# Performance work log

Measured on AMD Instinct MI355X. Metric: run time of the kernel, lower is better.

The kernel has to match this reference:

```python
import jax, jax.numpy as jnp
import numpy as np

HEADS = 4
EPS_LN = 1e-5
EPS_NORM = 1e-12

def conv1x1(x, w):
    # x: [B,C,T,H,W], w: [O,C] (Conv3d kernel_size=1, no bias)
    return jnp.einsum('oc,bcthw->bothw', w, x)

def dwconv3(x, w):
    # depthwise Conv3d 3x3x3, padding=1; w: [C,1,3,3,3]
    return jax.lax.conv_general_dilated(
        x, w, window_strides=(1, 1, 1), padding='SAME',
        dimension_numbers=('NCDHW', 'OIDHW', 'NCDHW'),
        feature_group_count=x.shape[1])

def layernorm_c(x, w, b):
    # LayerNorm over channel dim (torch LN applied after b c t h w -> b (thw) c)
    m = jnp.mean(x, axis=1, keepdims=True)
    v = jnp.mean(jnp.square(x - m), axis=1, keepdims=True)
    xn = (x - m) * jax.lax.rsqrt(v + EPS_LN)
    return xn * w[None, :, None, None, None] + b[None, :, None, None, None]

def l2norm(x):
    n = jnp.sqrt(jnp.sum(jnp.square(x), axis=-1, keepdims=True))
    return x / jnp.maximum(n, EPS_NORM)

def attention_c(x, qkv_w, qkv_dw_w, proj_w, temperature):
    B, C, T, H, W = x.shape
    qkv = dwconv3(conv1x1(x, qkv_w), qkv_dw_w)  # [B,3C,T,H,W]
    q, k, v = jnp.split(qkv, 3, axis=1)
    def to_heads(a):
        return a.reshape(B, HEADS, C // HEADS, T * H * W)  # b head c (thw)
    q, k, v = to_heads(q), to_heads(k), to_heads(v)
    q = l2norm(q)
    k = l2norm(k)
    # channel attention: [b,h,c,c] score matrix scaled by learnable temperature
    attn = jnp.einsum('bhcn,bhdn->bhcd', q, k) * temperature[None]
    attn = jax.nn.softmax(attn, axis=-1)
    out = jnp.einsum('bhcd,bhdn->bhcn', attn, v)
    out = out.reshape(B, C, T, H, W)
    return conv1x1(out, proj_w)

def feedforward(x, pin_w, ffn_dw_w, pout_w):
    h = conv1x1(x, pin_w)            # [B,2H,T,H,W]
    h = dwconv3(h, ffn_dw_w)
    x1, x2 = jnp.split(h, 2, axis=1)
    g = jax.nn.gelu(x1, approximate=False) * x2
    return conv1x1(g, pout_w)

def setup_inputs() -> dict:
    key = jax.random.key(0)
    ks = jax.random.split(key, 8)
    C, T, H, W = 192, 10, 64, 64
    Hf = int(C * 2.66)  # 510
    s = 0.05
    return {
        'x': jax.random.normal(ks[0], (1, C, T, H, W), jnp.float32),
        'ln1_w': jnp.ones((C,), jnp.float32),
        'ln1_b': jnp.zeros((C,), jnp.float32),
        'qkv_w': jax.random.normal(ks[1], (3 * C, C), jnp.float32) * s,
        'qkv_dw_w': jax.random.normal(ks[2], (3 * C, 1, 3, 3, 3), jnp.float32) * s,
        'proj_w': jax.random.normal(ks[3], (C, C), jnp.float32) * s,
        'temperature': jnp.ones((HEADS, 1, 1), jnp.float32),
        'ln2_w': jnp.ones((C,), jnp.float32),
        'ln2_b': jnp.zeros((C,), jnp.float32),
        'pin_w': jax.random.normal(ks[4], (2 * Hf, C), jnp.float32) * s,
        'ffn_dw_w': jax.random.normal(ks[5], (2 * Hf, 1, 3, 3, 3), jnp.float32) * s,
        'pout_w': jax.random.normal(ks[6], (C, Hf), jnp.float32) * s,
    }

def reference(x, ln1_w, ln1_b, qkv_w, qkv_dw_w, proj_w, temperature,
              ln2_w, ln2_b, pin_w, ffn_dw_w, pout_w):
    y = x + attention_c(layernorm_c(x, ln1_w, ln1_b), qkv_w, qkv_dw_w, proj_w, temperature)
    out = y + feedforward(layernorm_c(y, ln2_w, ln2_b), pin_w, ffn_dw_w, pout_w)
    return out
```

## Files before the change

### kernel.cpp

```cpp
#include <hip/hip_runtime.h>
#include <math.h>

#define NPOS 40960
#define TT 10
#define HH 64
#define WW 64
#define HWP 4096
#define CIN 192
#define C3 576
#define NHEADS 4
#define CHD 48
#define HF 510
#define GNB 80
#define GCHUNK 512

typedef unsigned short u16;
typedef unsigned int   u32;
typedef __bf16 bf16x8 __attribute__((ext_vector_type(8)));
typedef __bf16 bf16x2 __attribute__((ext_vector_type(2)));
typedef float  f32x4  __attribute__((ext_vector_type(4)));
typedef u16    u16x8  __attribute__((ext_vector_type(8)));
typedef u32    u32x4  __attribute__((ext_vector_type(4)));

__device__ __forceinline__ float b2f(u16 u) {
    return __uint_as_float(((unsigned int)u) << 16);
}
__device__ __forceinline__ u16 f2b(float f) {
    unsigned int i = __float_as_uint(f);
    unsigned int r = (i + 0x7FFFu + ((i >> 16) & 1u)) >> 16;
    return (u16)r;
}
__device__ __forceinline__ u16 f2bh(float f) {
    return __builtin_bit_cast(u16, static_cast<__bf16>(f));
}
__device__ __forceinline__ float gelu_exact(float v) {
    return 0.5f * v * (1.0f + erff(v * 0.70710678118654752f));
}

__device__ __forceinline__ float dot2bf(u32 a, u32 b, float c) {
#if __has_builtin(__builtin_amdgcn_fdot2_f32_bf16)
    return __builtin_amdgcn_fdot2_f32_bf16(
        __builtin_bit_cast(bf16x2, a), __builtin_bit_cast(bf16x2, b), c, false);
#else
    float a0 = b2f((u16)(a & 0xffffu)), a1 = b2f((u16)(a >> 16));
    float b0 = b2f((u16)(b & 0xffffu)), b1 = b2f((u16)(b >> 16));
    return fmaf(a1, b1, fmaf(a0, b0, c));
#endif
}
__device__ __forceinline__ u32 alignp(u32 hi, u32 lo) {
#if __has_builtin(__builtin_amdgcn_alignbit)
    return __builtin_amdgcn_alignbit(hi, lo, 16);
#else
    return (lo >> 16) | (hi << 16);
#endif
}

#define GLD_LDS16(g, l) __builtin_amdgcn_global_load_lds( \
    (const __attribute__((address_space(1))) void*)(g), \
    (__attribute__((address_space(3))) void*)(l), 16, 0, 0)

#define CVT_N1 (640 * 192)
#define CVT_N2 (1024 * 192)
#define CVT_N3 (256 * 512)
__global__ void cvtw_k(const float* __restrict__ qkv_w, const float* __restrict__ pin_w,
                       const float* __restrict__ pout_w,
                       u16* __restrict__ qkv_wb, u16* __restrict__ pin_wb,
                       u16* __restrict__ pout_wb) {
    int idx = blockIdx.x * 256 + threadIdx.x;
    if (idx < CVT_N1) {
        int r = idx / 192, c = idx % 192;
        qkv_wb[idx] = f2bh(r < 576 ? qkv_w[r * 192 + c] : 0.f);
    } else if (idx < CVT_N1 + CVT_N2) {
        int k = idx - CVT_N1;
        int r = k / 192, c = k % 192;
        pin_wb[k] = f2bh(r < 1020 ? pin_w[r * 192 + c] : 0.f);
    } else if (idx < CVT_N1 + CVT_N2 + CVT_N3) {
        int k = idx - CVT_N1 - CVT_N2;
        int r = k / 512, c = k % 512;
        pout_wb[k] = f2bh((r < 192 && c < 510) ? pout_w[r * 510 + c] : 0.f);
    }
}

template<typename InT>
__global__ __launch_bounds__(256) void lnt_k(const InT* __restrict__ X,
                                             const float* __restrict__ w,
                                             const float* __restrict__ b,
                                             u16* __restrict__ Xt) {
    __shared__ float sm[CIN][65];
    __shared__ float ps[4][64], ps2[4][64];
    __shared__ float smean[64], srstd[64];
    __shared__ float sw[CIN], sb[CIN];
    const int tid = threadIdx.x;
    const int n0 = blockIdx.x * 64;
    if (tid < CIN) { sw[tid] = w[tid]; sb[tid] = b[tid]; }
    if constexpr (sizeof(InT) == 4) {
        #pragma unroll
        for (int i = 0; i < 12; ++i) {
            int e = i * 256 + tid;
            int c = e >> 4, p4 = (e & 15) * 4;
            float4 v = *(const float4*)((const float*)X + (size_t)c * NPOS + n0 + p4);
            sm[c][p4 + 0] = v.x; sm[c][p4 + 1] = v.y;
            sm[c][p4 + 2] = v.z; sm[c][p4 + 3] = v.w;
        }
    } else {
        #pragma unroll
        for (int i = 0; i < 6; ++i) {
            int e = i * 256 + tid;
            int c = e >> 3, p8 = (e & 7) * 8;
            u16x8 v = *(const u16x8*)((const u16*)X + (size_t)c * NPOS + n0 + p8);
            #pragma unroll
            for (int j = 0; j < 8; ++j) sm[c][p8 + j] = b2f(v[j]);
        }
    }
    __syncthreads();
    int g = tid >> 6, nn = tid & 63;
    float s = 0.f, s2 = 0.f;
    for (int c = g * 48; c < g * 48 + 48; ++c) {
        float v = sm[c][nn];
        s += v; s2 += v * v;
    }
    ps[g][nn] = s; ps2[g][nn] = s2;
    __syncthreads();
    if (g == 0) {
        float t = ps[0][nn] + ps[1][nn] + ps[2][nn] + ps[3][nn];
        float t2 = ps2[0][nn] + ps2[1][nn] + ps2[2][nn] + ps2[3][nn];
        float m = t / CIN;
        float var = t2 / CIN - m * m;
        smean[nn] = m;
        srstd[nn] = rsqrtf(var + 1e-5f);
    }
    __syncthreads();
    #pragma unroll
    for (int i = 0; i < 6; ++i) {
        int e = i * 256 + tid;
        int nl = e / 24, cg = e % 24;
        int c0 = cg * 8;
        float m = smean[nl], rs_ = srstd[nl];
        u16x8 o;
        #pragma unroll
        for (int j = 0; j < 8; ++j) {
            float v = (sm[c0 + j][nl] - m) * rs_ * sw[c0 + j] + sb[c0 + j];
            o[j] = f2bh(v);
        }
        *(u16x8*)(Xt + (size_t)(n0 + nl) * CIN + c0) = o;
    }
}

__global__ __launch_bounds__(256) void transpose_pad_k(const u16* __restrict__ src,
                                                       u16* __restrict__ dst,
                                                       int CS, int CD) {
    __shared__ float sm[64][65];
    const int tid = threadIdx.x;
    const int n0 = blockIdx.x * 64;
    const int cb = blockIdx.y * 64;
    #pragma unroll
    for (int i = 0; i < 2; ++i) {
        int e = i * 256 + tid;
        int cl = e >> 3, nn8 = (e & 7) * 8;
        int c = cb + cl;
        if (c < CS) {
            u16x8 v = *(const u16x8*)(src + (size_t)c * NPOS + n0 + nn8);
            #pragma unroll
            for (int j = 0; j < 8; ++j) sm[cl][nn8 + j] = b2f(v[j]);
        } else {
            #pragma unroll
            for (int j = 0; j < 8; ++j) sm[cl][nn8 + j] = 0.f;
        }
    }
    __syncthreads();
    #pragma unroll
    for (int i = 0; i < 2; ++i) {
        int e = i * 256 + tid;
        int nl = e >> 3, c0 = (e & 7) * 8;
        u16x8 o;
        #pragma unroll
        for (int j = 0; j < 8; ++j) o[j] = f2bh(sm[c0 + j][nl]);
        *(u16x8*)(dst + (size_t)(n0 + nl) * CD + cb + c0) = o;
    }
}

template<int KP, typename OutT, typename ResT, bool RESID>
__global__ __launch_bounds__(256) void gemm_mfma_k(
    const u16* __restrict__ A, const u16* __restrict__ Bt, int O,
    const ResT* __restrict__ resid, OutT* __restrict__ outp)
{
    constexpr int NT = KP / 32;
    __shared__ u16 As[2][128 * 32];
    __shared__ u16 Bs[2][128 * 32];
    const int tid  = threadIdx.x;
    const int lane = tid & 63;
    const int wv   = tid >> 6;
    const int lo = lane & 15, hi = lane >> 4;
    const int m_blk = blockIdx.y * 128;
    const int n_blk = blockIdx.x * 128;

    int bb0 = (0 * 4 + wv) * 1024 + lane * 16;
    int bb1 = (1 * 4 + wv) * 1024 + lane * 16;
    const int r0 = bb0 >> 6, c80 = (bb0 >> 4) & 3;
    const int r1 = bb1 >> 6, c81 = (bb1 >> 4) & 3;

    auto stage = [&](int buf, int k0) {
        GLD_LDS16(A  + (size_t)(m_blk + r0) * KP + k0 + c80 * 8, (char*)&As[buf][0] + (0 * 4 + wv) * 1024);
        GLD_LDS16(A  + (size_t)(m_blk + r1) * KP + k0 + c81 * 8, (char*)&As[buf][0] + (1 * 4 + wv) * 1024);
        GLD_LDS16(Bt + (size_t)(n_blk + r0) * KP + k0 + c80 * 8, (char*)&Bs[buf][0] + (0 * 4 + wv) * 1024);
        GLD_LDS16(Bt + (size_t)(n_blk + r1) * KP + k0 + c81 * 8, (char*)&Bs[buf][0] + (1 * 4 + wv) * 1024);
    };

    f32x4 acc[4][4];
    const f32x4 zero = {0.f, 0.f, 0.f, 0.f};
    #pragma unroll
    for (int mt = 0; mt < 4; ++mt)
        #pragma unroll
        for (int nt = 0; nt < 4; ++nt) acc[mt][nt] = zero;

    stage(0, 0);
    __syncthreads();

    #pragma unroll
    for (int t = 0; t < NT; ++t) {
        if (t + 1 < NT) stage((t + 1) & 1, (t + 1) * 32);
        const u16* Ab = &As[t & 1][0] + (wv & 1) * 64 * 32;
        const u16* Bb = &Bs[t & 1][0] + (wv >> 1) * 64 * 32;
        bf16x8 a[4], b[4];
        #pragma unroll
        for (int q = 0; q < 4; ++q) {
            a[q] = *(const bf16x8*)(Ab + (q * 16 + lo) * 32 + hi * 8);
            b[q] = *(const bf16x8*)(Bb + (q * 16 + lo) * 32 + hi * 8);
        }
        #pragma unroll
        for (int mt = 0; mt < 4; ++mt)
            #pragma unroll
            for (int nt = 0; nt < 4; ++nt)
                acc[mt][nt] = __builtin_amdgcn_mfma_f32_16x16x32_bf16(
                    a[mt], b[nt], acc[mt][nt], 0, 0, 0);
        __syncthreads();
    }

    const int m_base = m_blk + (wv & 1) * 64;
    const int n_base = n_blk + (wv >> 1) * 64;
    #pragma unroll
    for (int mt = 0; mt < 4; ++mt) {
        #pragma unroll
        for (int r = 0; r < 4; ++r) {
            int m = m_base + mt * 16 + hi * 4 + r;
            if (m < O) {
                size_t rowoff = (size_t)m * NPOS;
                #pragma unroll
                for (int nt = 0; nt < 4; ++nt) {
                    int n = n_base + nt * 16 + lo;
                    float v = acc[mt][nt][r];
                    if (RESID) {
                        if constexpr (sizeof(ResT) == 2) v += b2f(((const u16*)resid)[rowoff + n]);
                        else                             v += ((const float*)resid)[rowoff + n];
                    }
                    if constexpr (sizeof(OutT) == 2) outp[rowoff + n] = (OutT)f2bh(v);
                    else                             outp[rowoff + n] = (OutT)v;
                }
            }
        }
    }
}

__global__ __launch_bounds__(256) void dwconv_k(const u16* __restrict__ in,
                                                u16* __restrict__ outp,
                                                const float* __restrict__ wgt,
                                                float* __restrict__ nrm2)
{
    __shared__ float red[256];
    const int lane = threadIdx.x & 63;
    const int wv   = threadIdx.x >> 6;
    const int c    = blockIdx.x >> 1;
    const int hb   = blockIdx.x & 1;
    const int h    = hb * 32 + wv * 8 + (lane >> 3);
    const int w0c  = (lane & 7) * 8;
    const bool wl0 = (lane & 7) == 0;
    const bool wl7 = (lane & 7) == 7;
    const bool hup = (h > 0), hdn = (h < HH - 1);
    u32 W01[9], W2h[9];
    {
        const float* wc = wgt + c * 27;
        #pragma unroll
        for (int i = 0; i < 9; ++i) {
            float a = wc[i * 3 + 0], b = wc[i * 3 + 1], d = wc[i * 3 + 2];
            W01[i] = (u32)f2b(a) | ((u32)f2b(b) << 16);
            W2h[i] = ((u32)f2b(d)) << 16;
        }
    }
    const u16* base = in   + (size_t)c * (TT * HWP);
    u16*       ob   = outp + (size_t)c * (TT * HWP);

    u32x4 zv = {0u, 0u, 0u, 0u};
    u32x4 ld[2][3];
    auto issue = [&](int ph, int ts) {
        const u16* rp = base + (size_t)ts * HWP + h * WW + w0c;
        ld[ph][0] = hup ? *(const u32x4*)(rp - WW) : zv;
        ld[ph][1] = *(const u32x4*)(rp);
        ld[ph][2] = hdn ? *(const u32x4*)(rp + WW) : zv;
    };

    float acc[3][8];
    #pragma unroll
    for (int o_ = 0; o_ < 3; ++o_)
        #pragma unroll
        for (int j = 0; j < 8; ++j) acc[o_][j] = 0.f;
    float sq = 0.f;

    issue(0, 0);
    #pragma unroll
    for (int ts = 0; ts < TT; ++ts) {
        const int cb = ts & 1, nb = cb ^ 1;
        if (ts + 1 < TT) issue(nb, ts + 1);
        #pragma unroll
        for (int dh = 0; dh < 3; ++dh) {
            u32 P0 = ld[cb][dh][0], P1 = ld[cb][dh][1];
            u32 P2 = ld[cb][dh][2], P3 = ld[cb][dh][3];
            u32 Pm = __shfl(P3, lane - 1); Pm = wl0 ? 0u : Pm;
            u32 Pp = __shfl(P0, lane + 1); Pp = wl7 ? 0u : Pp;
            u32 S0 = alignp(P0, Pm), S1 = alignp(P1, P0);
            u32 S2 = alignp(P2, P1), S3 = alignp(P3, P2);
            u32 S4 = alignp(Pp, P3);
            #pragma unroll
            for (int tp = 0; tp < 3; ++tp) {
                int o_;
                if (tp == 2) { if (ts < 1) continue; o_ = (ts - 1) % 3; }
                else if (tp == 1) { o_ = ts % 3; }
                else { if (ts + 1 >= TT) continue; o_ = (ts + 1) % 3; }
                const u32 wA = W01[tp * 3 + dh], wB = W2h[tp * 3 + dh];
                float* ap = acc[o_];
                ap[0] = dot2bf(S0, wA, ap[0]); ap[0] = dot2bf(P0, wB, ap[0]);
                ap[1] = dot2bf(P0, wA, ap[1]); ap[1] = dot2bf(S1, wB, ap[1]);
                ap[2] = dot2bf(S1, wA, ap[2]); ap[2] = dot2bf(P1, wB, ap[2]);
                ap[3] = dot2bf(P1, wA, ap[3]); ap[3] = dot2bf(S2, wB, ap[3]);
                ap[4] = dot2bf(S2, wA, ap[4]); ap[4] = dot2bf(P2, wB, ap[4]);
                ap[5] = dot2bf(P2, wA, ap[5]); ap[5] = dot2bf(S3, wB, ap[5]);
                ap[6] = dot2bf(S3, wA, ap[6]); ap[6] = dot2bf(P3, wB, ap[6]);
                ap[7] = dot2bf(P3, wA, ap[7]); ap[7] = dot2bf(S4, wB, ap[7]);
            }
        }
        if (ts >= 1) {
            const int o_ = (ts - 1) % 3;
            u16x8 o;
            #pragma unroll
            for (int j = 0; j < 8; ++j) {
                float v = acc[o_][j];
                sq = fmaf(v, v, sq);
                o[j] = f2bh(v);
            }
            *(u16x8*)(ob + (size_t)(ts - 1) * HWP + h * WW + w0c) = o;
            #pragma unroll
            for (int j = 0; j < 8; ++j) acc[o_][j] = 0.f;
        }
    }
    {
        const int o_ = (TT - 1) % 3;
        u16x8 o;
        #pragma unroll
        for (int j = 0; j < 8; ++j) {
            float v = acc[o_][j];
            sq = fmaf(v, v, sq);
            o[j] = f2bh(v);
        }
        *(u16x8*)(ob + (size_t)(TT - 1) * HWP + h * WW + w0c) = o;
    }
    if (nrm2) {
        red[threadIdx.x] = sq;
        __syncthreads();
        for (int off = 128; off > 0; off >>= 1) {
            if (threadIdx.x < off) red[threadIdx.x] += red[threadIdx.x + off];
            __syncthreads();
        }
        if (threadIdx.x == 0) nrm2[c * 2 + hb] = red[0];
    }
}

__global__ __launch_bounds__(256) void dwconv_glu_k(const u16* __restrict__ in,
                                                    u16* __restrict__ gout,
                                                    const float* __restrict__ wgt)
{
    const int lane = threadIdx.x & 63;
    const int wv   = threadIdx.x >> 6;
    const int c    = blockIdx.x >> 1;
    const int hb   = blockIdx.x & 1;
    const int h    = hb * 32 + wv * 8 + (lane >> 3);
    const int w0c  = (lane & 7) * 8;
    const bool wl0 = (lane & 7) == 0;
    const bool wl7 = (lane & 7) == 7;
    const bool hup = (h > 0), hdn = (h < HH - 1);

    u32 W01[2][9], W2h[2][9];
    #pragma unroll
    for (int ch = 0; ch < 2; ++ch) {
        const float* wc = wgt + (size_t)(c + ch * HF) * 27;
        #pragma unroll
        for (int i = 0; i < 9; ++i) {
            float a = wc[i * 3 + 0], b = wc[i * 3 + 1], d = wc[i * 3 + 2];
            W01[ch][i] = (u32)f2b(a) | ((u32)f2b(b) << 16);
            W2h[ch][i] = ((u32)f2b(d)) << 16;
        }
    }
    const u16* base0 = in + (size_t)c * (TT * HWP);
    const u16* base1 = in + (size_t)(c + HF) * (TT * HWP);
    u16* ob = gout + (size_t)c * (TT * HWP);

    u32x4 zv = {0u, 0u, 0u, 0u};
    u32x4 ld[2][2][3];
    auto issue = [&](int ph, int ts) {
        const u16* rp0 = base0 + (size_t)ts * HWP + h * WW + w0c;
        ld[0][ph][0] = hup ? *(const u32x4*)(rp0 - WW) : zv;
        ld[0][ph][1] = *(const u32x4*)(rp0);
        ld[0][ph][2] = hdn ? *(const u32x4*)(rp0 + WW) : zv;
        const u16* rp1 = base1 + (size_t)ts * HWP + h * WW + w0c;
        ld[1][ph][0] = hup ? *(const u32x4*)(rp1 - WW) : zv;
        ld[1][ph][1] = *(const u32x4*)(rp1);
        ld[1][ph][2] = hdn ? *(const u32x4*)(rp1 + WW) : zv;
    };

    float acc[2][3][8];
    #pragma unroll
    for (int ch = 0; ch < 2; ++ch)
        #pragma unroll
        for (int o_ = 0; o_ < 3; ++o_)
            #pragma unroll
            for (int j = 0; j < 8; ++j) acc[ch][o_][j] = 0.f;

    issue(0, 0);
    #pragma unroll
    for (int ts = 0; ts < TT; ++ts) {
        const int cb = ts & 1, nb = cb ^ 1;
        if (ts + 1 < TT) issue(nb, ts + 1);
        #pragma unroll
        for (int ch = 0; ch < 2; ++ch) {
            #pragma unroll
            for (int dh = 0; dh < 3; ++dh) {
                u32 P0 = ld[ch][cb][dh][0], P1 = ld[ch][cb][dh][1];
                u32 P2 = ld[ch][cb][dh][2], P3 = ld[ch][cb][dh][3];
                u32 Pm = __shfl(P3, lane - 1); Pm = wl0 ? 0u : Pm;
                u32 Pp = __shfl(P0, lane + 1); Pp = wl7 ? 0u : Pp;
                u32 S0 = alignp(P0, Pm), S1 = alignp(P1, P0);
                u32 S2 = alignp(P2, P1), S3 = alignp(P3, P2);
                u32 S4 = alignp(Pp, P3);
                #pragma unroll
                for (int tp = 0; tp < 3; ++tp) {
                    int o_;
                    if (tp == 2) { if (ts < 1) continue; o_ = (ts - 1) % 3; }
                    else if (tp == 1) { o_ = ts % 3; }
                    else { if (ts + 1 >= TT) continue; o_ = (ts + 1) % 3; }
                    const u32 wA = W01[ch][tp * 3 + dh], wB = W2h[ch][tp * 3 + dh];
                    float* ap = acc[ch][o_];
                    ap[0] = dot2bf(S0, wA, ap[0]); ap[0] = dot2bf(P0, wB, ap[0]);
                    ap[1] = dot2bf(P0, wA, ap[1]); ap[1] = dot2bf(S1, wB, ap[1]);
                    ap[2] = dot2bf(S1, wA, ap[2]); ap[2] = dot2bf(P1, wB, ap[2]);
                    ap[3] = dot2bf(P1, wA, ap[3]); ap[3] = dot2bf(S2, wB, ap[3]);
                    ap[4] = dot2bf(S2, wA, ap[4]); ap[4] = dot2bf(P2, wB, ap[4]);
                    ap[5] = dot2bf(P2, wA, ap[5]); ap[5] = dot2bf(S3, wB, ap[5]);
                    ap[6] = dot2bf(S3, wA, ap[6]); ap[6] = dot2bf(P3, wB, ap[6]);
                    ap[7] = dot2bf(P3, wA, ap[7]); ap[7] = dot2bf(S4, wB, ap[7]);
                }
            }
        }
        if (ts >= 1) {
            const int o_ = (ts - 1) % 3;
            u16x8 o;
            #pragma unroll
            for (int j = 0; j < 8; ++j)
                o[j] = f2bh(gelu_exact(acc[0][o_][j]) * acc[1][o_][j]);
            *(u16x8*)(ob + (size_t)(ts - 1) * HWP + h * WW + w0c) = o;
            #pragma unroll
            for (int j = 0; j < 8; ++j) { acc[0][o_][j] = 0.f; acc[1][o_][j] = 0.f; }
        }
    }
    {
        const int o_ = (TT - 1) % 3;
        u16x8 o;
        #pragma unroll
        for (int j = 0; j < 8; ++j)
            o[j] = f2bh(gelu_exact(acc[0][o_][j]) * acc[1][o_][j]);
        *(u16x8*)(ob + (size_t)(TT - 1) * HWP + h * WW + w0c) = o;
    }
}

__global__ __launch_bounds__(64) void gram_k(const u16* __restrict__ qkv,
                                             float* __restrict__ part) {
    const int h  = blockIdx.x / GNB;
    const int nb = blockIdx.x % GNB;
    const int lane = threadIdx.x;
    const int lo = lane & 15, hi = lane >> 4;
    const u16* qp = qkv + (size_t)(h * CHD) * NPOS + (size_t)nb * GCHUNK + hi * 8;
    const u16* kp = qkv + (size_t)(CIN + h * CHD) * NPOS + (size_t)nb * GCHUNK + hi * 8;
    f32x4 acc[3][3];
    const f32x4 zero = {0.f, 0.f, 0.f, 0.f};
    #pragma unroll
    for (int mt = 0; mt < 3; ++mt)
        #pragma unroll
        for (int nt = 0; nt < 3; ++nt) acc[mt][nt] = zero;
    #pragma unroll
    for (int ks = 0; ks < GCHUNK; ks += 32) {
        bf16x8 a[3], b[3];
        #pragma unroll
        for (int t = 0; t < 3; ++t) {
            a[t] = *(const bf16x8*)(qp + (size_t)(t * 16 + lo) * NPOS + ks);
            b[t] = *(const bf16x8*)(kp + (size_t)(t * 16 + lo) * NPOS + ks);
        }
        #pragma unroll
        for (int mt = 0; mt < 3; ++mt)
            #pragma unroll
            for (int nt = 0; nt < 3; ++nt)
                acc[mt][nt] = __builtin_amdgcn_mfma_f32_16x16x32_bf16(
                    a[mt], b[nt], acc[mt][nt], 0, 0, 0);
    }
    float* pp = part + (size_t)blockIdx.x * 2304;
    #pragma unroll
    for (int mt = 0; mt < 3; ++mt)
        #pragma unroll
        for (int nt = 0; nt < 3; ++nt)
            #pragma unroll
            for (int r = 0; r < 4; ++r)
                pp[(mt * 16 + hi * 4 + r) * 48 + nt * 16 + lo] = acc[mt][nt][r];
}

__global__ void gram_reduce_k(const float* __restrict__ part, float* __restrict__ S) {
    int idx = blockIdx.x * blockDim.x + threadIdx.x;
    if (idx >= NHEADS * 2304) return;
    int h = idx / 2304, cd = idx % 2304;
    float s = 0.f;
    for (int nb = 0; nb < GNB; ++nb) s += part[(size_t)(h * GNB + nb) * 2304 + cd];
    S[idx] = s;
}

__global__ void softmax_k(const float* __restrict__ S, const float* __restrict__ norm2p,
                          const float* __restrict__ temp, float* __restrict__ attn) {
    int row = threadIdx.x;
    if (row >= 192) return;
    int h = row / CHD;
    float qn = fmaxf(sqrtf(norm2p[2 * row] + norm2p[2 * row + 1]), 1e-12f);
    float t = temp[h];
    float vals[48];
    float mx = -1e30f;
    for (int d = 0; d < CHD; ++d) {
        int kc = CIN + h * CHD + d;
        float kn = fmaxf(sqrtf(norm2p[2 * kc] + norm2p[2 * kc + 1]), 1e-12f);
        float v = t * S[row * CHD + d] / (qn * kn);
        vals[d] = v; mx = fmaxf(mx, v);
    }
    float sum = 0.f;
    for (int d = 0; d < CHD; ++d) { float e = expf(vals[d] - mx); vals[d] = e; sum += e; }
    float inv = 1.f / sum;
    for (int d = 0; d < CHD; ++d) attn[row * CHD + d] = vals[d] * inv;
}

__global__ void mmat_k(const float* __restrict__ proj_w, const float* __restrict__ attn,
                       u16* __restrict__ Mb) {
    int idx = blockIdx.x * blockDim.x + threadIdx.x;
    if (idx >= 256 * CIN) return;
    int o = idx / CIN, j = idx % CIN;
    float s = 0.f;
    if (o < CIN) {
        int h = j / CHD, d = j % CHD;
        for (int c = 0; c < CHD; ++c)
            s += proj_w[o * CIN + h * CHD + c] * attn[(h * CHD + c) * CHD + d];
    }
    Mb[idx] = f2bh(s);
}

extern "C" void kernel_launch(void* const* d_in, const int* in_sizes, int n_in,
                              void* d_out, int out_size, void* d_ws, size_t ws_size,
                              hipStream_t stream) {
    const float* x       = (const float*)d_in[0];
    const float* ln1w    = (const float*)d_in[1];
    const float* ln1b    = (const float*)d_in[2];
    const float* qkv_w   = (const float*)d_in[3];
    const float* qkv_dw  = (const float*)d_in[4];
    const float* proj_w  = (const float*)d_in[5];
    const float* temp    = (const float*)d_in[6];
    const float* ln2w    = (const float*)d_in[7];
    const float* ln2b    = (const float*)d_in[8];
    const float* pin_w   = (const float*)d_in[9];
    const float* ffn_dw  = (const float*)d_in[10];
    const float* pout_w  = (const float*)d_in[11];
    float* out = (float*)d_out;

    char* wsb = (char*)d_ws;
    size_t off = 0;
    auto alloc = [&](size_t bytes) {
        void* p = wsb + off; off += (bytes + 255) & ~(size_t)255; return p;
    };
    float* norm2p  = (float*)alloc(C3 * 2 * 4);
    float* Sbuf    = (float*)alloc(NHEADS * 2304 * 4);
    float* attn    = (float*)alloc(NHEADS * 2304 * 4);
    float* part    = (float*)alloc((size_t)NHEADS * GNB * 2304 * 4);
    u16*   qkv_wb  = (u16*)alloc((size_t)640 * 192 * 2);
    u16*   pin_wb  = (u16*)alloc((size_t)1024 * 192 * 2);
    u16*   pout_wb = (u16*)alloc((size_t)256 * 512 * 2);
    u16*   M_b     = (u16*)alloc((size_t)256 * 192 * 2);
    u16*   xn1_t   = (u16*)alloc((size_t)NPOS * 192 * 2);
    u16*   yn2_t   = (u16*)alloc((size_t)NPOS * 192 * 2);
    u16*   ybuf    = (u16*)alloc((size_t)CIN * NPOS * 2);
    u16*   regionA = (u16*)alloc((size_t)1024 * NPOS * 2);
    u16*   regionB = (u16*)alloc((size_t)1024 * NPOS * 2);
    u16* qkv_raw  = regionA;
    u16* qkv_conv = regionB;
    u16* h_raw    = regionA;
    u16* g510     = regionB;
    u16* gt       = regionA;
    u16* vt       = xn1_t;

    cvtw_k<<<(CVT_N1 + CVT_N2 + CVT_N3 + 255) / 256, 256, 0, stream>>>(
        qkv_w, pin_w, pout_w, qkv_wb, pin_wb, pout_wb);
    lnt_k<float><<<NPOS / 64, 256, 0, stream>>>(x, ln1w, ln1b, xn1_t);
    gemm_mfma_k<192, u16, float, false><<<dim3(NPOS / 128, 5), 256, 0, stream>>>(
        qkv_wb, xn1_t, C3, nullptr, qkv_raw);
    dwconv_k<<<C3 * 2, 256, 0, stream>>>(qkv_raw, qkv_conv, qkv_dw, norm2p);
    gram_k<<<NHEADS * GNB, 64, 0, stream>>>(qkv_conv, part);
    gram_reduce_k<<<(NHEADS * 2304 + 255) / 256, 256, 0, stream>>>(part, Sbuf);
    softmax_k<<<1, 192, 0, stream>>>(Sbuf, norm2p, temp, attn);
    mmat_k<<<(256 * CIN + 255) / 256, 256, 0, stream>>>(proj_w, attn, M_b);
    transpose_pad_k<<<dim3(NPOS / 64, 3), 256, 0, stream>>>(
        qkv_conv + (size_t)384 * NPOS, vt, 192, 192);
    gemm_mfma_k<192, u16, float, true><<<dim3(NPOS / 128, 2), 256, 0, stream>>>(
        M_b, vt, CIN, x, ybuf);
    lnt_k<u16><<<NPOS / 64, 256, 0, stream>>>(ybuf, ln2w, ln2b, yn2_t);
    gemm_mfma_k<192, u16, float, false><<<dim3(NPOS / 128, 8), 256, 0, stream>>>(
        pin_wb, yn2_t, 1024, nullptr, h_raw);
    dwconv_glu_k<<<HF * 2, 256, 0, stream>>>(h_raw, g510, ffn_dw);
    transpose_pad_k<<<dim3(NPOS / 64, 8), 256, 0, stream>>>(g510, gt, HF, 512);
    gemm_mfma_k<512, float, u16, true><<<dim3(NPOS / 128, 2), 256, 0, stream>>>(
        pout_wb, gt, CIN, ybuf, out);
}
```

Measured before the change: 252.5 us.

## Split GLU depthwise conv channels across waves and combine via shared memory

The FFN depthwise-conv+GLU kernel previously had each thread compute both the gelu and the gate channel. Now each block has 512 threads: four waves compute the gelu half and four waves the gate half. The gelu results are exchanged through a double-buffered LDS tile and combined by the gate waves before writing. This halves per-thread registers and doubles the number of waves for latency hiding, at the cost of a block-wide barrier per time step and extra LDS traffic.

```diff
diff --git a/kernel.cpp b/kernel.cpp
--- a/kernel.cpp
+++ b/kernel.cpp
@@ -373,55 +373,73 @@
     }
 }
 
-__global__ __launch_bounds__(256) void dwconv_glu_k(const u16* __restrict__ in,
-                                                    u16* __restrict__ gout,
-                                                    const float* __restrict__ wgt)
+__global__ __launch_bounds__(512, 8) void dwconv_glu2_k(const u16* __restrict__ in,
+                                                        u16* __restrict__ gout,
+                                                        const float* __restrict__ wgt)
 {
-    const int lane = threadIdx.x & 63;
-    const int wv   = threadIdx.x >> 6;
-    const int c    = blockIdx.x >> 1;
+    __shared__ float gbuf[2][32][66];
+    const int tid  = threadIdx.x;
+    const int lane = tid & 63;
+    const int wv   = tid >> 6;
+    const int ch   = wv >> 2;
+    const int wvc  = wv & 3;
+    const int cpr  = blockIdx.x >> 1;
     const int hb   = blockIdx.x & 1;
-    const int h    = hb * 32 + wv * 8 + (lane >> 3);
+    const int hr   = wvc * 8 + (lane >> 3);
+    const int h    = hb * 32 + hr;
     const int w0c  = (lane & 7) * 8;
     const bool wl0 = (lane & 7) == 0;
     const bool wl7 = (lane & 7) == 7;
     const bool hup = (h > 0), hdn = (h < HH - 1);
 
-    u32 W01[2][9], W2h[2][9];
-    #pragma unroll
-    for (int ch = 0; ch < 2; ++ch) {
-        const float* wc = wgt + (size_t)(c + ch * HF) * 27;
+    const int cc = __builtin_amdgcn_readfirstlane(cpr + ch * HF);
+    u32 W01[9], W2h[9];
+    {
+        const float* wc = wgt + (size_t)cc * 27;
         #pragma unroll
         for (int i = 0; i < 9; ++i) {
             float a = wc[i * 3 + 0], b = wc[i * 3 + 1], d = wc[i * 3 + 2];
-            W01[ch][i] = (u32)f2b(a) | ((u32)f2b(b) << 16);
-            W2h[ch][i] = ((u32)f2b(d)) << 16;
-        }
-    }
-    const u16* base0 = in + (size_t)c * (TT * HWP);
-    const u16* base1 = in + (size_t)(c + HF) * (TT * HWP);
-    u16* ob = gout + (size_t)c * (TT * HWP);
+            W01[i] = (u32)f2b(a) | ((u32)f2b(b) << 16);
+            W2h[i] = ((u32)f2b(d)) << 16;
+        }
+    }
+    const u16* base = in + (size_t)cc * (TT * HWP);
+    u16* ob = gout + (size_t)cpr * (TT * HWP);
 
     u32x4 zv = {0u, 0u, 0u, 0u};
-    u32x4 ld[2][2][3];
+    u32x4 ld[2][3];
     auto issue = [&](int ph, int ts) {
-        const u16* rp0 = base0 + (size_t)ts * HWP + h * WW + w0c;
-        ld[0][ph][0] = hup ? *(const u32x4*)(rp0 - WW) : zv;
-        ld[0][ph][1] = *(const u32x4*)(rp0);
-        ld[0][ph][2] = hdn ? *(const u32x4*)(rp0 + WW) : zv;
-        const u16* rp1 = base1 + (size_t)ts * HWP + h * WW + w0c;
-        ld[1][ph][0] = hup ? *(const u32x4*)(rp1 - WW) : zv;
-        ld[1][ph][1] = *(const u32x4*)(rp1);
-        ld[1][ph][2] = hdn ? *(const u32x4*)(rp1 + WW) : zv;
+        const u16* rp = base + (size_t)ts * HWP + h * WW + w0c;
+        ld[ph][0] = hup ? *(const u32x4*)(rp - WW) : zv;
+        ld[ph][1] = *(const u32x4*)(rp);
+        ld[ph][2] = hdn ? *(const u32x4*)(rp + WW) : zv;
     };
 
-    float acc[2][3][8];
-    #pragma unroll
-    for (int ch = 0; ch < 2; ++ch)
-        #pragma unroll
-        for (int o_ = 0; o_ < 3; ++o_)
-            #pragma unroll
-            for (int j = 0; j < 8; ++j) acc[ch][o_][j] = 0.f;
+    float acc[3][8];
+    #pragma unroll
+    for (int o_ = 0; o_ < 3; ++o_)
+        #pragma unroll
+        for (int j = 0; j < 8; ++j) acc[o_][j] = 0.f;
+
+    auto emit = [&](int ots) {
+        const int o_ = ots % 3;
+        const int bf = ots & 1;
+        if (ch == 0) {
+            #pragma unroll
+            for (int j = 0; j < 8; ++j)
+                gbuf[bf][hr][w0c + j] = gelu_exact(acc[o_][j]);
+        }
+        __syncthreads();
+        if (ch == 1) {
+            u16x8 o;
+            #pragma unroll
+            for (int j = 0; j < 8; ++j)
+                o[j] = f2bh(gbuf[bf][hr][w0c + j] * acc[o_][j]);
+            *(u16x8*)(ob + (size_t)ots * HWP + h * WW + w0c) = o;
+        }
+        #pragma unroll
+        for (int j = 0; j < 8; ++j) acc[o_][j] = 0.f;
+    };
 
     issue(0, 0);
     #pragma unroll
@@ -429,54 +447,35 @@
         const int cb = ts & 1, nb = cb ^ 1;
         if (ts + 1 < TT) issue(nb, ts + 1);
         #pragma unroll
-        for (int ch = 0; ch < 2; ++ch) {
-            #pragma unroll
-            for (int dh = 0; dh < 3; ++dh) {
-                u32 P0 = ld[ch][cb][dh][0], P1 = ld[ch][cb][dh][1];
-                u32 P2 = ld[ch][cb][dh][2], P3 = ld[ch][cb][dh][3];
-                u32 Pm = __shfl(P3, lane - 1); Pm = wl0 ? 0u : Pm;
-                u32 Pp = __shfl(P0, lane + 1); Pp = wl7 ? 0u : Pp;
-                u32 S0 = alignp(P0, Pm), S1 = alignp(P1, P0);
-                u32 S2 = alignp(P2, P1), S3 = alignp(P3, P2);
-                u32 S4 = alignp(Pp, P3);
-                #pragma unroll
-                for (int tp = 0; tp < 3; ++tp) {
-                    int o_;
-                    if (tp == 2) { if (ts < 1) continue; o_ = (ts - 1) % 3; }
-                    else if (tp == 1) { o_ = ts % 3; }
-                    else { if (ts + 1 >= TT) continue; o_ = (ts + 1) % 3; }
-                    const u32 wA = W01[ch][tp * 3 + dh], wB = W2h[ch][tp * 3 + dh];
-                    float* ap = acc[ch][o_];
-                    ap[0] = dot2bf(S0, wA, ap[0]); ap[0] = dot2bf(P0, wB, ap[0]);
-                    ap[1] = dot2bf(P0, wA, ap[1]); ap[1] = dot2bf(S1, wB, ap[1]);
-                    ap[2] = dot2bf(S1, wA, ap[2]); ap[2] = dot2bf(P1, wB, ap[2]);
-                    ap[3] = dot2bf(P1, wA, ap[3]); ap[3] = dot2bf(S2, wB, ap[3]);
-                    ap[4] = dot2bf(S2, wA, ap[4]); ap[4] = dot2bf(P2, wB, ap[4]);
-                    ap[5] = dot2bf(P2, wA, ap[5]); ap[5] = dot2bf(S3, wB, ap[5]);
-                    ap[6] = dot2bf(S3, wA, ap[6]); ap[6] = dot2bf(P3, wB, ap[6]);
-                    ap[7] = dot2bf(P3, wA, ap[7]); ap[7] = dot2bf(S4, wB, ap[7]);
-                }
+        for (int dh = 0; dh < 3; ++dh) {
+            u32 P0 = ld[cb][dh][0], P1 = ld[cb][dh][1];
+            u32 P2 = ld[cb][dh][2], P3 = ld[cb][dh][3];
+            u32 Pm = __shfl(P3, lane - 1); Pm = wl0 ? 0u : Pm;
+            u32 Pp = __shfl(P0, lane + 1); Pp = wl7 ? 0u : Pp;
+            u32 S0 = alignp(P0, Pm), S1 = alignp(P1, P0);
+            u32 S2 = alignp(P2, P1), S3 = alignp(P3, P2);
+            u32 S4 = alignp(Pp, P3);
+            #pragma unroll
+            for (int tp = 0; tp < 3; ++tp) {
+                int o_;
+                if (tp == 2) { if (ts < 1) continue; o_ = (ts - 1) % 3; }
+                else if (tp == 1) { o_ = ts % 3; }
+                else { if (ts + 1 >= TT) continue; o_ = (ts + 1) % 3; }
+                const u32 wA = W01[tp * 3 + dh], wB = W2h[tp * 3 + dh];
+                float* ap = acc[o_];
+                ap[0] = dot2bf(S0, wA, ap[0]); ap[0] = dot2bf(P0, wB, ap[0]);
+                ap[1] = dot2bf(P0, wA, ap[1]); ap[1] = dot2bf(S1, wB, ap[1]);
+                ap[2] = dot2bf(S1, wA, ap[2]); ap[2] = dot2bf(P1, wB, ap[2]);
+                ap[3] = dot2bf(P1, wA, ap[3]); ap[3] = dot2bf(S2, wB, ap[3]);
+                ap[4] = dot2bf(S2, wA, ap[4]); ap[4] = dot2bf(P2, wB, ap[4]);
+                ap[5] = dot2bf(P2, wA, ap[5]); ap[5] = dot2bf(S3, wB, ap[5]);
+                ap[6] = dot2bf(S3, wA, ap[6]); ap[6] = dot2bf(P3, wB, ap[6]);
+                ap[7] = dot2bf(P3, wA, ap[7]); ap[7] = dot2bf(S4, wB, ap[7]);
             }
         }
-        if (ts >= 1) {
-            const int o_ = (ts - 1) % 3;
-            u16x8 o;
-            #pragma unroll
-            for (int j = 0; j < 8; ++j)
-                o[j] = f2bh(gelu_exact(acc[0][o_][j]) * acc[1][o_][j]);
-            *(u16x8*)(ob + (size_t)(ts - 1) * HWP + h * WW + w0c) = o;
-            #pragma unroll
-            for (int j = 0; j < 8; ++j) { acc[0][o_][j] = 0.f; acc[1][o_][j] = 0.f; }
-        }
-    }
-    {
-        const int o_ = (TT - 1) % 3;
-        u16x8 o;
-        #pragma unroll
-        for (int j = 0; j < 8; ++j)
-            o[j] = f2bh(gelu_exact(acc[0][o_][j]) * acc[1][o_][j]);
-        *(u16x8*)(ob + (size_t)(TT - 1) * HWP + h * WW + w0c) = o;
-    }
+        if (ts >= 1) emit(ts - 1);
+    }
+    emit(TT - 1);
 }
 
 __global__ __launch_bounds__(64) void gram_k(const u16* __restrict__ qkv,
@@ -621,7 +620,7 @@
     lnt_k<u16><<<NPOS / 64, 256, 0, stream>>>(ybuf, ln2w, ln2b, yn2_t);
     gemm_mfma_k<192, u16, float, false><<<dim3(NPOS / 128, 8), 256, 0, stream>>>(
         pin_wb, yn2_t, 1024, nullptr, h_raw);
-    dwconv_glu_k<<<HF * 2, 256, 0, stream>>>(h_raw, g510, ffn_dw);
+    dwconv_glu2_k<<<HF * 2, 512, 0, stream>>>(h_raw, g510, ffn_dw);
     transpose_pad_k<<<dim3(NPOS / 64, 8), 256, 0, stream>>>(g510, gt, HF, 512);
     gemm_mfma_k<512, float, u16, true><<<dim3(NPOS / 128, 2), 256, 0, stream>>>(
         pout_wb, gt, CIN, ybuf, out);
```

Result: slower. 347.7 us (+37.7%).
